# Optimization experiments

Measured on AMD Instinct MI355X. Metric: run time of the kernel, lower is better.

The kernel has to match this reference:

```python
import jax, jax.numpy as jnp
import numpy as np

N_NODES = 50000
N_EDGES = 640000
RAW = 128
HID = 256
COORD = 3


def setup_inputs() -> dict:
    key = jax.random.key(0)
    ks = jax.random.split(key, 20)

    def w(k, fan_in, fan_out):
        return (jax.random.normal(k, (fan_in, fan_out), jnp.float32)
                / np.float32(np.sqrt(fan_in)))

    return {
        "edge_index": jax.random.randint(ks[0], (2, N_EDGES), 0, N_NODES, jnp.int64)
        if jax.config.jax_enable_x64 else
        jax.random.randint(ks[0], (2, N_EDGES), 0, N_NODES, jnp.int32),
        "str_feature": jax.random.normal(ks[1], (N_NODES, RAW), jnp.float32),
        "coord_feature": jax.random.normal(ks[2], (N_NODES, COORD), jnp.float32),
        # msg_mlp: Linear(2*RAW+1 -> HID), SiLU, Linear(HID -> HID), SiLU
        "msg_w1": w(ks[3], 2 * RAW + 1, HID), "msg_b1": jnp.zeros((HID,), jnp.float32),
        "msg_w2": w(ks[4], HID, HID), "msg_b2": jnp.zeros((HID,), jnp.float32),
        # trans_mlp: Linear(HID->HID), SiLU, Linear(HID->HID), SiLU, Linear(HID->1, no bias, xavier gain=0.001)
        "tr_w1": w(ks[5], HID, HID), "tr_b1": jnp.zeros((HID,), jnp.float32),
        "tr_w2": w(ks[6], HID, HID), "tr_b2": jnp.zeros((HID,), jnp.float32),
        "tr_w3": w(ks[7], HID, 1) * np.float32(0.001),
        # posi_mlp: Linear(RAW+HID->HID), SiLU, Linear(HID->RAW)
        "posi_w1": w(ks[8], RAW + HID, HID), "posi_b1": jnp.zeros((HID,), jnp.float32),
        "posi_w2": w(ks[9], HID, RAW), "posi_b2": jnp.zeros((RAW,), jnp.float32),
    }


def reference(edge_index, str_feature, coord_feature,
              msg_w1, msg_b1, msg_w2, msg_b2,
              tr_w1, tr_b1, tr_w2, tr_b2, tr_w3,
              posi_w1, posi_b1, posi_w2, posi_b2):
    silu = jax.nn.silu
    row, col = edge_index[0], edge_index[1]
    n = str_feature.shape[0]

    # coord2dist
    coord_diff = coord_feature[row] - coord_feature[col]          # [E, 3]
    sqr_dist = jnp.sum(coord_diff * coord_diff, axis=1, keepdims=True)  # [E, 1]

    # msg_model
    edge_in = jnp.concatenate([str_feature[row], str_feature[col], sqr_dist], axis=1)
    msg = silu(silu(edge_in @ msg_w1 + msg_b1) @ msg_w2 + msg_b2)  # [E, HID]

    # coord_model: trans = coord_diff * trans_mlp(msg); x += segment_mean(trans, row)
    gate = silu(silu(msg @ tr_w1 + tr_b1) @ tr_w2 + tr_b2) @ tr_w3  # [E, 1]
    trans = coord_diff * gate                                       # [E, 3]
    trans_sum = jax.ops.segment_sum(trans, row, num_segments=n)     # [N, 3]
    cnt = jax.ops.segment_sum(jnp.ones((trans.shape[0],), trans.dtype), row,
                              num_segments=n)
    trans_mean = trans_sum / jnp.clip(cnt, 1.0)[:, None]
    coord_out = coord_feature + trans_mean

    # posi_model: p + posi_mlp([p, segment_sum(msg, row)])
    msg_sum = jax.ops.segment_sum(msg, row, num_segments=n)         # [N, HID]
    p_in = jnp.concatenate([str_feature, msg_sum], axis=1)
    str_out = str_feature + (silu(p_in @ posi_w1 + posi_b1) @ posi_w2 + posi_b2)

    return str_out, coord_out
```

## Files before the change

kernel.cpp:

```cpp
#include <hip/hip_runtime.h>

#define NN 50000
#define NE 640000

typedef __bf16 bf16x8 __attribute__((ext_vector_type(8)));
typedef short  short8 __attribute__((ext_vector_type(8)));
typedef float  f32x16 __attribute__((ext_vector_type(16)));
typedef float  f32x2  __attribute__((ext_vector_type(2)));
typedef float  f32x4  __attribute__((ext_vector_type(4)));

__device__ __forceinline__ short f2bf(float v) {
  unsigned u = __builtin_bit_cast(unsigned, v);
  u = (u + 0x7FFFu + ((u >> 16) & 1u)) >> 16;
  return (short)u;
}
__device__ __forceinline__ short f2bf_hw(float v) {
  return __builtin_bit_cast(short, (__bf16)v);
}
__device__ __forceinline__ float silu_f(float v) {
  float e = __builtin_amdgcn_exp2f(v * -1.44269504f);
  return v * __builtin_amdgcn_rcpf(1.0f + e);
}
__device__ __forceinline__ bf16x8 ld8(const short* p) {
  return *(const bf16x8*)(p);
}
__device__ __forceinline__ void atomic_add_f(float* p, float v) {
  __hip_atomic_fetch_add(p, v, __ATOMIC_RELAXED, __HIP_MEMORY_SCOPE_AGENT);
}

__global__ void egcl_prep(const float* __restrict__ mw1, const float* __restrict__ mb1,
                          const float* __restrict__ mw2, const float* __restrict__ mb2,
                          const float* __restrict__ tw1, const float* __restrict__ tb1,
                          const float* __restrict__ tw2, const float* __restrict__ tb2,
                          const float* __restrict__ pw1, const float* __restrict__ pw2,
                          const float* __restrict__ strf, const int* __restrict__ rowp,
                          short* __restrict__ w1t, short* __restrict__ w2t,
                          short* __restrict__ t1t, short* __restrict__ t2t,
                          short* __restrict__ p1t, short* __restrict__ p2t,
                          short* __restrict__ strb, int* __restrict__ deg)
{
  const int S0 = 71680, S2 = 98304, S3 = 32768, SS = NN * 128;
  const int total = 4 * S0 + S2 + S3 + SS + NE;
  int stride = gridDim.x * blockDim.x;
  for (int i = blockIdx.x * blockDim.x + threadIdx.x; i < total; i += stride) {
    int j = i;
    if (j < S0) { int n = j / 280, k = j - n * 280;
      float v = (k < 257) ? mw1[k * 256 + n] : ((k == 257) ? mb1[n] : 0.0f);
      w1t[j] = f2bf(v); continue; }
    j -= S0;
    if (j < S0) { int n = j / 280, k = j - n * 280;
      float v = (k < 256) ? mw2[k * 256 + n] : ((k == 257) ? mb2[n] : 0.0f);
      w2t[j] = f2bf(v); continue; }
    j -= S0;
    if (j < S0) { int n = j / 280, k = j - n * 280;
      float v = (k < 256) ? tw1[k * 256 + n] : ((k == 257) ? tb1[n] : 0.0f);
      t1t[j] = f2bf(v); continue; }
    j -= S0;
    if (j < S0) { int n = j / 280, k = j - n * 280;
      float v = (k < 256) ? tw2[k * 256 + n] : ((k == 257) ? tb2[n] : 0.0f);
      t2t[j] = f2bf(v); continue; }
    j -= S0;
    if (j < S2) { int n = j / 384, k = j - n * 384; p1t[j] = f2bf(pw1[k * 256 + n]); continue; }
    j -= S2;
    if (j < S3) { int n = j >> 8, k = j & 255; p2t[j] = f2bf(pw2[k * 128 + n]); continue; }
    j -= S3;
    if (j < SS) { strb[j] = f2bf(strf[j]); continue; }
    j -= SS;
    atomicAdd(deg + rowp[j], 1);
  }
}

__global__ __launch_bounds__(1024)
void egcl_scan(const int* __restrict__ deg, int* __restrict__ base)
{
  __shared__ int wsum[16], wincl[16];
  __shared__ int carry_s;
  const int tid = threadIdx.x, lane = tid & 63, w = tid >> 6;
  if (tid == 0) carry_s = 0;
  __syncthreads();
  for (int start = 0; start < NN; start += 1024) {
    const int i = start + tid;
    int v = (i < NN) ? deg[i] : 0;
    int s = v;
#pragma unroll
    for (int off = 1; off < 64; off <<= 1) {
      int t = __shfl_up(s, off);
      if (lane >= off) s += t;
    }
    if (lane == 63) wsum[w] = s;
    __syncthreads();
    if (w == 0) {
      int u = (lane < 16) ? wsum[lane] : 0;
#pragma unroll
      for (int off = 1; off < 16; off <<= 1) {
        int t = __shfl_up(u, off);
        if (lane >= off) u += t;
      }
      if (lane < 16) wincl[lane] = u;
    }
    __syncthreads();
    const int waveoff = wincl[w] - wsum[w];
    const int carry = carry_s;
    if (i < NN) base[i] = carry + waveoff + s - v;
    __syncthreads();
    if (tid == 0) carry_s = carry + wincl[15];
    __syncthreads();
  }
  if (tid == 0) base[NN] = NE;
}

__global__ void egcl_scatter(const int* __restrict__ rowp, const int* __restrict__ base,
                             int* __restrict__ cursor, int* __restrict__ eidg)
{
  int stride = gridDim.x * blockDim.x;
  for (int e = blockIdx.x * blockDim.x + threadIdx.x; e < NE; e += stride) {
    int r = rowp[e];
    int pos = base[r] + atomicAdd(cursor + r, 1);
    eidg[pos] = e;
  }
}


template<int NKS>
__device__ __forceinline__ void gemm64(const short* Ab, const short* __restrict__ WT,
                                       int wn, int lh, int l32, f32x16 acc[4])
{
  acc[0] = (f32x16)(0.0f); acc[1] = (f32x16)(0.0f);
  acc[2] = (f32x16)(0.0f); acc[3] = (f32x16)(0.0f);
  const short* arow = Ab + l32 * 280 + lh * 8;
  const short* brow = WT + (wn * 64 + l32) * 280 + lh * 8;
#pragma unroll
  for (int ks = 0; ks < NKS; ++ks) {
    const int kb = ks * 16;
    bf16x8 b0 = ld8(brow + kb);
    bf16x8 b1 = ld8(brow + 32 * 280 + kb);
    bf16x8 a0 = ld8(arow + kb);
    bf16x8 a1 = ld8(arow + 32 * 280 + kb);
    acc[0] = __builtin_amdgcn_mfma_f32_32x32x16_bf16(a0, b0, acc[0], 0, 0, 0);
    acc[1] = __builtin_amdgcn_mfma_f32_32x32x16_bf16(a1, b0, acc[1], 0, 0, 0);
    acc[2] = __builtin_amdgcn_mfma_f32_32x32x16_bf16(a0, b1, acc[2], 0, 0, 0);
    acc[3] = __builtin_amdgcn_mfma_f32_32x32x16_bf16(a1, b1, acc[3], 0, 0, 0);
  }
}

__device__ __forceinline__ void silu_acc(f32x16 acc[4], float b0, float b1)
{
#pragma unroll
  for (int i = 0; i < 4; ++i) {
    const float b = (i < 2) ? b0 : b1;
#pragma unroll
    for (int r = 0; r < 16; ++r) acc[i][r] = silu_f(acc[i][r] + b);
  }
}

__device__ __forceinline__ void write_acc(short* Ab, const f32x16 acc[4],
                                          int wn, int lh, int l32)
{
#pragma unroll
  for (int nh = 0; nh < 2; ++nh) {
    const int n = wn * 64 + nh * 32 + l32;
#pragma unroll
    for (int sm = 0; sm < 2; ++sm) {
      const f32x16& a = acc[nh * 2 + sm];
      short* dst = Ab + (sm * 32 + 4 * lh) * 280 + n;
#pragma unroll
      for (int j = 0; j < 8; ++j) {
        const int row = (j & 1) * 2 + 8 * (j >> 1);
        dst[row * 280]       = f2bf_hw(a[2 * j]);
        dst[(row + 1) * 280] = f2bf_hw(a[2 * j + 1]);
      }
    }
  }
}

__global__ __launch_bounds__(256, 4)
void egcl_edge(const int* __restrict__ eidx, const float* __restrict__ coord,
               const short* __restrict__ strb, const int* __restrict__ eidg,
               const int* __restrict__ base,
               const short* __restrict__ w1t, const short* __restrict__ w2t,
               const short* __restrict__ t1t, const short* __restrict__ t2t,
               const float* __restrict__ mb2v, const float* __restrict__ tb1v,
               const float* __restrict__ tb2v,
               const float* __restrict__ tr_w3,
               float* __restrict__ msg_sum, float* __restrict__ trans_sum)
{
  __shared__ short Ab[64 * 280];
  __shared__ int   rs_s[64], own_s[64];
  __shared__ float cdx_s[64], cdy_s[64], cdz_s[64], gate_s[64];

  const int tid  = threadIdx.x;
  const int lane = tid & 63, wave = tid >> 6;
  const int lh = lane >> 5, l32 = lane & 31;
  const int wn = wave;
  const int p0 = blockIdx.x * 64;
  const int* __restrict__ rowp = eidx;
  const int* __restrict__ colp = eidx + NE;

  const int nb = wn * 64 + l32;
  const float b2_0 = mb2v[nb], b2_1 = mb2v[nb + 32];
  const float b3_0 = tb1v[nb], b3_1 = tb1v[nb + 32];
  const float b4_0 = tb2v[nb], b4_1 = tb2v[nb + 32];

  if (tid < 64) {
    int e = eidg[p0 + tid];
    int r = rowp[e], c = colp[e];
    rs_s[tid] = r;
    const int wstart = p0 + (tid & ~31);
    own_s[tid] = (base[r] >= wstart) && (base[r + 1] <= wstart + 32) ? 1 : 0;
    float dx = coord[r * 3 + 0] - coord[c * 3 + 0];
    float dy = coord[r * 3 + 1] - coord[c * 3 + 1];
    float dz = coord[r * 3 + 2] - coord[c * 3 + 2];
    cdx_s[tid] = dx; cdy_s[tid] = dy; cdz_s[tid] = dz;
    short8 d8 = (short8)(short)0;
    d8[0] = f2bf(dx * dx + dy * dy + dz * dz);
    d8[1] = f2bf(1.0f);
    *(short8*)(Ab + tid * 280 + 256) = d8;
    *(short8*)(Ab + tid * 280 + 264) = (short8)(short)0;
    *(short8*)(Ab + tid * 280 + 272) = (short8)(short)0;
  }
#pragma unroll
  for (int it = 0; it < 8; ++it) {
    int i = tid + it * 256;
    int e = i >> 5, cc = i & 31;
    int eid = eidg[p0 + e];
    int node = (cc < 16) ? rowp[eid] : colp[eid];
    short8 v = *(const short8*)(strb + node * 128 + (cc & 15) * 8);
    *(short8*)(Ab + e * 280 + cc * 8) = v;
  }
  __syncthreads();

  f32x16 acc[4];

  gemm64<17>(Ab, w1t, wn, lh, l32, acc);
  silu_acc(acc, 0.0f, 0.0f);
  __syncthreads();
  write_acc(Ab, acc, wn, lh, l32);
  __syncthreads();

  gemm64<16>(Ab, w2t, wn, lh, l32, acc);
  silu_acc(acc, b2_0, b2_1);
  __syncthreads();
  write_acc(Ab, acc, wn, lh, l32);
  __syncthreads();

  gemm64<16>(Ab, t1t, wn, lh, l32, acc);
  silu_acc(acc, b3_0, b3_1);
  {
    const int cp  = tid & 127;
    const int e0w = (tid >> 7) * 32;
    float run0 = 0.0f, run1 = 0.0f;
    int prev = rs_s[e0w];
    int own  = own_s[e0w];
#pragma unroll 4
    for (int i = 0; i < 32; ++i) {
      const int idx = e0w + i;
      const int r = rs_s[idx];
      unsigned u = *(const unsigned*)(Ab + idx * 280 + cp * 2);
      float lo = __builtin_bit_cast(float, u << 16);
      float hi = __builtin_bit_cast(float, u & 0xFFFF0000u);
      if (r != prev) {
        if (own) {
          f32x2 v; v.x = run0; v.y = run1;
          *((f32x2*)msg_sum + prev * 128 + cp) = v;
        } else {
          atomic_add_f(msg_sum + prev * 256 + cp * 2 + 0, run0);
          atomic_add_f(msg_sum + prev * 256 + cp * 2 + 1, run1);
        }
        run0 = 0.0f; run1 = 0.0f; prev = r; own = own_s[idx];
      }
      run0 += lo; run1 += hi;
    }
    if (own) {
      f32x2 v; v.x = run0; v.y = run1;
      *((f32x2*)msg_sum + prev * 128 + cp) = v;
    } else {
      atomic_add_f(msg_sum + prev * 256 + cp * 2 + 0, run0);
      atomic_add_f(msg_sum + prev * 256 + cp * 2 + 1, run1);
    }
  }
  __syncthreads();
  write_acc(Ab, acc, wn, lh, l32);
  __syncthreads();

  gemm64<16>(Ab, t2t, wn, lh, l32, acc);
  silu_acc(acc, b4_0, b4_1);
  __syncthreads();
  write_acc(Ab, acc, wn, lh, l32);
  __syncthreads();

  {
    const int e = tid >> 2, p = tid & 3;
    const short* ap = Ab + e * 280 + p * 64;
    const float4* wp = (const float4*)(tr_w3 + p * 64);
    float s = 0.0f;
#pragma unroll
    for (int j = 0; j < 8; ++j) {
      bf16x8 av = ld8(ap + j * 8);
      float4 w0 = wp[2 * j], w1 = wp[2 * j + 1];
      s += (float)av[0] * w0.x + (float)av[1] * w0.y + (float)av[2] * w0.z + (float)av[3] * w0.w;
      s += (float)av[4] * w1.x + (float)av[5] * w1.y + (float)av[6] * w1.z + (float)av[7] * w1.w;
    }
    s += __shfl_xor(s, 1);
    s += __shfl_xor(s, 2);
    if (p == 0) gate_s[e] = s;
  }
  __syncthreads();
  if (tid < 64) {
    const int r = rs_s[tid];
    const float g = gate_s[tid];
    float vx = cdx_s[tid] * g, vy = cdy_s[tid] * g, vz = cdz_s[tid] * g;
#pragma unroll
    for (int off = 1; off < 64; off <<= 1) {
      int   rr = __shfl_up(r, off);
      float tx = __shfl_up(vx, off);
      float ty = __shfl_up(vy, off);
      float tz = __shfl_up(vz, off);
      if (tid >= off && rr == r) { vx += tx; vy += ty; vz += tz; }
    }
    int rn = __shfl_down(r, 1);
    if (tid == 63 || rn != r) {
      atomic_add_f(trans_sum + r * 3 + 0, vx);
      atomic_add_f(trans_sum + r * 3 + 1, vy);
      atomic_add_f(trans_sum + r * 3 + 2, vz);
    }
  }
}

__global__ __launch_bounds__(256, 3)
void egcl_node(const float* __restrict__ strf, const float* __restrict__ coord,
               const short* __restrict__ strb,
               const short* __restrict__ p1t, const short* __restrict__ p2t,
               const float* __restrict__ pb1, const float* __restrict__ pb2,
               const float* __restrict__ msg_sum, const float* __restrict__ trans_sum,
               const int* __restrict__ base, float* __restrict__ out)
{
  __shared__ short Ab[64 * 392];
  const int tid  = threadIdx.x;
  const int lane = tid & 63, wave = tid >> 6;
  const int quad = lane >> 4, l16 = lane & 15;
  const int n0 = blockIdx.x * 64;

#pragma unroll
  for (int it = 0; it < 4; ++it) {
    int i = tid + it * 256;
    int m = i >> 4, c = i & 15;
    int n = n0 + m;
    short8 v = (short8)(short)0;
    if (n < NN) v = *(const short8*)(strb + n * 128 + c * 8);
    *(short8*)(Ab + m * 392 + c * 8) = v;
  }
#pragma unroll
  for (int it = 0; it < 8; ++it) {
    int i = tid + it * 256;
    int m = i >> 5, c = i & 31;
    int n = n0 + m;
    short8 v = (short8)(short)0;
    if (n < NN) {
      const float* src = msg_sum + n * 256 + c * 8;
#pragma unroll
      for (int j = 0; j < 8; ++j) v[j] = f2bf_hw(src[j]);
    }
    *(short8*)(Ab + m * 392 + 128 + c * 8) = v;
  }
  __syncthreads();

  f32x4 acc[4][4];
#pragma unroll
  for (int nt = 0; nt < 4; ++nt)
#pragma unroll
    for (int mt = 0; mt < 4; ++mt) acc[nt][mt] = (f32x4)(0.0f);
#pragma unroll
  for (int ks = 0; ks < 12; ++ks) {
    const int kb = ks * 32 + quad * 8;
    bf16x8 b[4];
#pragma unroll
    for (int nt = 0; nt < 4; ++nt)
      b[nt] = ld8(p1t + (wave * 64 + nt * 16 + l16) * 384 + kb);
#pragma unroll
    for (int mt = 0; mt < 4; ++mt) {
      bf16x8 a = ld8(Ab + (mt * 16 + l16) * 392 + kb);
#pragma unroll
      for (int nt = 0; nt < 4; ++nt)
        acc[nt][mt] = __builtin_amdgcn_mfma_f32_16x16x32_bf16(a, b[nt], acc[nt][mt], 0, 0, 0);
    }
  }
  __syncthreads();
#pragma unroll
  for (int nt = 0; nt < 4; ++nt) {
    const int n = wave * 64 + nt * 16 + l16;
    const float bn = pb1[n];
#pragma unroll
    for (int mt = 0; mt < 4; ++mt)
#pragma unroll
      for (int r = 0; r < 4; ++r) {
        const int m = mt * 16 + quad * 4 + r;
        Ab[m * 392 + n] = f2bf_hw(silu_f(acc[nt][mt][r] + bn));
      }
  }
  __syncthreads();

  f32x4 a2[2][4];
#pragma unroll
  for (int nt = 0; nt < 2; ++nt)
#pragma unroll
    for (int mt = 0; mt < 4; ++mt) a2[nt][mt] = (f32x4)(0.0f);
#pragma unroll
  for (int ks = 0; ks < 8; ++ks) {
    const int kb = ks * 32 + quad * 8;
    bf16x8 b0 = ld8(p2t + (wave * 32 + l16) * 256 + kb);
    bf16x8 b1 = ld8(p2t + (wave * 32 + 16 + l16) * 256 + kb);
#pragma unroll
    for (int mt = 0; mt < 4; ++mt) {
      bf16x8 a = ld8(Ab + (mt * 16 + l16) * 392 + kb);
      a2[0][mt] = __builtin_amdgcn_mfma_f32_16x16x32_bf16(a, b0, a2[0][mt], 0, 0, 0);
      a2[1][mt] = __builtin_amdgcn_mfma_f32_16x16x32_bf16(a, b1, a2[1][mt], 0, 0, 0);
    }
  }
#pragma unroll
  for (int nt = 0; nt < 2; ++nt) {
    const int c = wave * 32 + nt * 16 + l16;
    const float bc = pb2[c];
#pragma unroll
    for (int mt = 0; mt < 4; ++mt)
#pragma unroll
      for (int r = 0; r < 4; ++r) {
        const int m = mt * 16 + quad * 4 + r;
        const int n = n0 + m;
        if (n < NN) out[n * 128 + c] = strf[n * 128 + c] + a2[nt][mt][r] + bc;
      }
  }
  if (tid < 64) {
    const int n = n0 + tid;
    if (n < NN) {
      float cv = (float)(base[n + 1] - base[n]); if (cv < 1.0f) cv = 1.0f;
      float inv = __builtin_amdgcn_rcpf(cv);
      out[NN * 128 + n * 3 + 0] = coord[n * 3 + 0] + trans_sum[n * 3 + 0] * inv;
      out[NN * 128 + n * 3 + 1] = coord[n * 3 + 1] + trans_sum[n * 3 + 1] * inv;
      out[NN * 128 + n * 3 + 2] = coord[n * 3 + 2] + trans_sum[n * 3 + 2] * inv;
    }
  }
}

extern "C" void kernel_launch(void* const* d_in, const int* in_sizes, int n_in,
                              void* d_out, int out_size, void* d_ws, size_t ws_size,
                              hipStream_t stream)
{
  const int*   eidx   = (const int*)d_in[0];
  const float* strf   = (const float*)d_in[1];
  const float* coord  = (const float*)d_in[2];
  const float* msg_w1 = (const float*)d_in[3];
  const float* msg_b1 = (const float*)d_in[4];
  const float* msg_w2 = (const float*)d_in[5];
  const float* msg_b2 = (const float*)d_in[6];
  const float* tr_w1  = (const float*)d_in[7];
  const float* tr_b1  = (const float*)d_in[8];
  const float* tr_w2  = (const float*)d_in[9];
  const float* tr_b2  = (const float*)d_in[10];
  const float* tr_w3  = (const float*)d_in[11];
  const float* posi_w1 = (const float*)d_in[12];
  const float* posi_b1 = (const float*)d_in[13];
  const float* posi_w2 = (const float*)d_in[14];
  const float* posi_b2 = (const float*)d_in[15];
  float* out = (float*)d_out;

  char* ws = (char*)d_ws;
  float* msg_sum   = (float*)ws;
  float* trans_sum = msg_sum + NN * 256;
  int*   deg       = (int*)(trans_sum + NN * 3);
  int*   cursor    = deg + NN;
  int*   base      = cursor + NN;
  int*   eidg      = base + NN + 8;
  short* strb = (short*)(eidg + NE);
  short* w1t  = strb + NN * 128;
  short* w2t  = w1t + 71680;
  short* t1t  = w2t + 71680;
  short* t2t  = t1t + 71680;
  short* p1t  = t2t + 71680;
  short* p2t  = p1t + 98304;

  const int* rowp = eidx;

  (void)hipMemsetAsync(ws, 0, (size_t)(NN * 256 + NN * 3 + NN + NN) * 4, stream);
  egcl_prep<<<2048, 256, 0, stream>>>(msg_w1, msg_b1, msg_w2, msg_b2,
                                      tr_w1, tr_b1, tr_w2, tr_b2,
                                      posi_w1, posi_w2,
                                      strf, rowp, w1t, w2t, t1t, t2t, p1t, p2t, strb, deg);
  egcl_scan<<<1, 1024, 0, stream>>>(deg, base);
  egcl_scatter<<<2560, 256, 0, stream>>>(rowp, base, cursor, eidg);
  egcl_edge<<<NE / 64, 256, 0, stream>>>(eidx, coord, strb, eidg, base,
                                         w1t, w2t, t1t, t2t,
                                         msg_b2, tr_b1, tr_b2, tr_w3,
                                         msg_sum, trans_sum);
  egcl_node<<<(NN + 63) / 64, 256, 0, stream>>>(strf, coord, strb, p1t, p2t,
                                                posi_b1, posi_b2,
                                                msg_sum, trans_sum, base, out);
}
```

Measured before the change: 1.040 ms.

## Retile edge MLP GEMMs to 2x2 waves with register-held A fragments

```diff
diff --git a/kernel.cpp b/kernel.cpp
--- a/kernel.cpp
+++ b/kernel.cpp
@@ -49,15 +49,15 @@
       w1t[j] = f2bf(v); continue; }
     j -= S0;
     if (j < S0) { int n = j / 280, k = j - n * 280;
-      float v = (k < 256) ? mw2[k * 256 + n] : ((k == 257) ? mb2[n] : 0.0f);
+      float v = (k < 256) ? mw2[k * 256 + n] : 0.0f;
       w2t[j] = f2bf(v); continue; }
     j -= S0;
     if (j < S0) { int n = j / 280, k = j - n * 280;
-      float v = (k < 256) ? tw1[k * 256 + n] : ((k == 257) ? tb1[n] : 0.0f);
+      float v = (k < 256) ? tw1[k * 256 + n] : 0.0f;
       t1t[j] = f2bf(v); continue; }
     j -= S0;
     if (j < S0) { int n = j / 280, k = j - n * 280;
-      float v = (k < 256) ? tw2[k * 256 + n] : ((k == 257) ? tb2[n] : 0.0f);
+      float v = (k < 256) ? tw2[k * 256 + n] : 0.0f;
       t2t[j] = f2bf(v); continue; }
     j -= S0;
     if (j < S2) { int n = j / 384, k = j - n * 384; p1t[j] = f2bf(pw1[k * 256 + n]); continue; }
@@ -122,58 +122,59 @@
 
 
 template<int NKS>
-__device__ __forceinline__ void gemm64(const short* Ab, const short* __restrict__ WT,
-                                       int wn, int lh, int l32, f32x16 acc[4])
+__device__ __forceinline__ void loadA(const short* Ab, int wm, int lh, int l32,
+                                      bf16x8 af[NKS])
+{
+  const short* arow = Ab + (wm * 32 + l32) * 280 + lh * 8;
+#pragma unroll
+  for (int ks = 0; ks < NKS; ++ks) af[ks] = ld8(arow + ks * 16);
+}
+
+template<int NKS>
+__device__ __forceinline__ void gemmA(const bf16x8 af[NKS], const short* __restrict__ WT,
+                                      int wn2, int lh, int l32, f32x16 acc[4])
 {
   acc[0] = (f32x16)(0.0f); acc[1] = (f32x16)(0.0f);
   acc[2] = (f32x16)(0.0f); acc[3] = (f32x16)(0.0f);
-  const short* arow = Ab + l32 * 280 + lh * 8;
-  const short* brow = WT + (wn * 64 + l32) * 280 + lh * 8;
+  const short* brow = WT + (wn2 * 128 + l32) * 280 + lh * 8;
 #pragma unroll
   for (int ks = 0; ks < NKS; ++ks) {
     const int kb = ks * 16;
     bf16x8 b0 = ld8(brow + kb);
     bf16x8 b1 = ld8(brow + 32 * 280 + kb);
-    bf16x8 a0 = ld8(arow + kb);
-    bf16x8 a1 = ld8(arow + 32 * 280 + kb);
-    acc[0] = __builtin_amdgcn_mfma_f32_32x32x16_bf16(a0, b0, acc[0], 0, 0, 0);
-    acc[1] = __builtin_amdgcn_mfma_f32_32x32x16_bf16(a1, b0, acc[1], 0, 0, 0);
-    acc[2] = __builtin_amdgcn_mfma_f32_32x32x16_bf16(a0, b1, acc[2], 0, 0, 0);
-    acc[3] = __builtin_amdgcn_mfma_f32_32x32x16_bf16(a1, b1, acc[3], 0, 0, 0);
-  }
-}
-
-__device__ __forceinline__ void silu_acc(f32x16 acc[4], float b0, float b1)
-{
-#pragma unroll
-  for (int i = 0; i < 4; ++i) {
-    const float b = (i < 2) ? b0 : b1;
-#pragma unroll
-    for (int r = 0; r < 16; ++r) acc[i][r] = silu_f(acc[i][r] + b);
-  }
-}
-
-__device__ __forceinline__ void write_acc(short* Ab, const f32x16 acc[4],
-                                          int wn, int lh, int l32)
-{
-#pragma unroll
-  for (int nh = 0; nh < 2; ++nh) {
-    const int n = wn * 64 + nh * 32 + l32;
-#pragma unroll
-    for (int sm = 0; sm < 2; ++sm) {
-      const f32x16& a = acc[nh * 2 + sm];
-      short* dst = Ab + (sm * 32 + 4 * lh) * 280 + n;
-#pragma unroll
-      for (int j = 0; j < 8; ++j) {
-        const int row = (j & 1) * 2 + 8 * (j >> 1);
-        dst[row * 280]       = f2bf_hw(a[2 * j]);
-        dst[(row + 1) * 280] = f2bf_hw(a[2 * j + 1]);
-      }
-    }
-  }
-}
-
-__global__ __launch_bounds__(256, 4)
+    bf16x8 b2 = ld8(brow + 64 * 280 + kb);
+    bf16x8 b3 = ld8(brow + 96 * 280 + kb);
+    acc[0] = __builtin_amdgcn_mfma_f32_32x32x16_bf16(af[ks], b0, acc[0], 0, 0, 0);
+    acc[1] = __builtin_amdgcn_mfma_f32_32x32x16_bf16(af[ks], b1, acc[1], 0, 0, 0);
+    acc[2] = __builtin_amdgcn_mfma_f32_32x32x16_bf16(af[ks], b2, acc[2], 0, 0, 0);
+    acc[3] = __builtin_amdgcn_mfma_f32_32x32x16_bf16(af[ks], b3, acc[3], 0, 0, 0);
+  }
+}
+
+__device__ __forceinline__ void siluD(f32x16 acc[4], const float bv[4])
+{
+#pragma unroll
+  for (int nc = 0; nc < 4; ++nc)
+#pragma unroll
+    for (int r = 0; r < 16; ++r) acc[nc][r] = silu_f(acc[nc][r] + bv[nc]);
+}
+
+__device__ __forceinline__ void writeD(short* Ab, const f32x16 acc[4],
+                                       int wm, int wn2, int lh, int l32)
+{
+#pragma unroll
+  for (int nc = 0; nc < 4; ++nc) {
+    short* dst = Ab + (wm * 32 + 4 * lh) * 280 + wn2 * 128 + nc * 32 + l32;
+#pragma unroll
+    for (int j = 0; j < 8; ++j) {
+      const int row = (j & 1) * 2 + 8 * (j >> 1);
+      dst[row * 280]       = f2bf_hw(acc[nc][2 * j]);
+      dst[(row + 1) * 280] = f2bf_hw(acc[nc][2 * j + 1]);
+    }
+  }
+}
+
+__global__ __launch_bounds__(256, 2)
 void egcl_edge(const int* __restrict__ eidx, const float* __restrict__ coord,
                const short* __restrict__ strb, const int* __restrict__ eidg,
                const int* __restrict__ base,
@@ -185,26 +186,31 @@
                float* __restrict__ msg_sum, float* __restrict__ trans_sum)
 {
   __shared__ short Ab[64 * 280];
-  __shared__ int   rs_s[64], own_s[64];
+  __shared__ int   rs_s[64], cs_s[64], own_s[64];
   __shared__ float cdx_s[64], cdy_s[64], cdz_s[64], gate_s[64];
 
   const int tid  = threadIdx.x;
   const int lane = tid & 63, wave = tid >> 6;
   const int lh = lane >> 5, l32 = lane & 31;
-  const int wn = wave;
+  const int wm = wave & 1, wn2 = wave >> 1;
   const int p0 = blockIdx.x * 64;
   const int* __restrict__ rowp = eidx;
   const int* __restrict__ colp = eidx + NE;
 
-  const int nb = wn * 64 + l32;
-  const float b2_0 = mb2v[nb], b2_1 = mb2v[nb + 32];
-  const float b3_0 = tb1v[nb], b3_1 = tb1v[nb + 32];
-  const float b4_0 = tb2v[nb], b4_1 = tb2v[nb + 32];
+  const int nb0 = wn2 * 128 + l32;
+  float b2v[4], b3v[4], b4v[4], zb[4];
+#pragma unroll
+  for (int nc = 0; nc < 4; ++nc) {
+    b2v[nc] = mb2v[nb0 + nc * 32];
+    b3v[nc] = tb1v[nb0 + nc * 32];
+    b4v[nc] = tb2v[nb0 + nc * 32];
+    zb[nc] = 0.0f;
+  }
 
   if (tid < 64) {
     int e = eidg[p0 + tid];
     int r = rowp[e], c = colp[e];
-    rs_s[tid] = r;
+    rs_s[tid] = r; cs_s[tid] = c;
     const int wstart = p0 + (tid & ~31);
     own_s[tid] = (base[r] >= wstart) && (base[r + 1] <= wstart + 32) ? 1 : 0;
     float dx = coord[r * 3 + 0] - coord[c * 3 + 0];
@@ -218,36 +224,41 @@
     *(short8*)(Ab + tid * 280 + 264) = (short8)(short)0;
     *(short8*)(Ab + tid * 280 + 272) = (short8)(short)0;
   }
+  __syncthreads();
 #pragma unroll
   for (int it = 0; it < 8; ++it) {
     int i = tid + it * 256;
     int e = i >> 5, cc = i & 31;
-    int eid = eidg[p0 + e];
-    int node = (cc < 16) ? rowp[eid] : colp[eid];
+    int node = (cc < 16) ? rs_s[e] : cs_s[e];
     short8 v = *(const short8*)(strb + node * 128 + (cc & 15) * 8);
     *(short8*)(Ab + e * 280 + cc * 8) = v;
   }
   __syncthreads();
 
+  bf16x8 af[17];
   f32x16 acc[4];
 
-  gemm64<17>(Ab, w1t, wn, lh, l32, acc);
-  silu_acc(acc, 0.0f, 0.0f);
-  __syncthreads();
-  write_acc(Ab, acc, wn, lh, l32);
-  __syncthreads();
-
-  gemm64<16>(Ab, w2t, wn, lh, l32, acc);
-  silu_acc(acc, b2_0, b2_1);
-  __syncthreads();
-  write_acc(Ab, acc, wn, lh, l32);
-  __syncthreads();
-
-  gemm64<16>(Ab, t1t, wn, lh, l32, acc);
-  silu_acc(acc, b3_0, b3_1);
+  loadA<17>(Ab, wm, lh, l32, af);
+  __syncthreads();
+  gemmA<17>(af, w1t, wn2, lh, l32, acc);
+  siluD(acc, zb);
+  writeD(Ab, acc, wm, wn2, lh, l32);
+  __syncthreads();
+
+  loadA<16>(Ab, wm, lh, l32, af);
+  __syncthreads();
+  gemmA<16>(af, w2t, wn2, lh, l32, acc);
+  siluD(acc, b2v);
+  writeD(Ab, acc, wm, wn2, lh, l32);
+  __syncthreads();
+
+  loadA<16>(Ab, wm, lh, l32, af);
+  __syncthreads();
+  gemmA<16>(af, t1t, wn2, lh, l32, acc);
+  siluD(acc, b3v);
   {
-    const int cp  = tid & 127;
-    const int e0w = (tid >> 7) * 32;
+    const int cp  = wn2 * 64 + lane;
+    const int e0w = wm * 32;
     float run0 = 0.0f, run1 = 0.0f;
     int prev = rs_s[e0w];
     int own  = own_s[e0w];
@@ -278,14 +289,14 @@
       atomic_add_f(msg_sum + prev * 256 + cp * 2 + 1, run1);
     }
   }
-  __syncthreads();
-  write_acc(Ab, acc, wn, lh, l32);
-  __syncthreads();
-
-  gemm64<16>(Ab, t2t, wn, lh, l32, acc);
-  silu_acc(acc, b4_0, b4_1);
-  __syncthreads();
-  write_acc(Ab, acc, wn, lh, l32);
+  writeD(Ab, acc, wm, wn2, lh, l32);
+  __syncthreads();
+
+  loadA<16>(Ab, wm, lh, l32, af);
+  __syncthreads();
+  gemmA<16>(af, t2t, wn2, lh, l32, acc);
+  siluD(acc, b4v);
+  writeD(Ab, acc, wm, wn2, lh, l32);
   __syncthreads();
 
   {
```

After: 1.348 ms. 29.7% more time.

## Shrink edge tile to 32 edges, pack bf16 outputs, fuse gate projection into epilogue

Applied to the files above, without the earlier changes.

```diff
diff --git a/kernel.cpp b/kernel.cpp
--- a/kernel.cpp
+++ b/kernel.cpp
@@ -17,6 +17,9 @@
 __device__ __forceinline__ short f2bf_hw(float v) {
   return __builtin_bit_cast(short, (__bf16)v);
 }
+__device__ __forceinline__ unsigned pack2(float a, float b) {
+  return (unsigned)(unsigned short)f2bf_hw(a) | ((unsigned)(unsigned short)f2bf_hw(b) << 16);
+}
 __device__ __forceinline__ float silu_f(float v) {
   float e = __builtin_amdgcn_exp2f(v * -1.44269504f);
   return v * __builtin_amdgcn_rcpf(1.0f + e);
@@ -29,9 +32,8 @@
 }
 
 __global__ void egcl_prep(const float* __restrict__ mw1, const float* __restrict__ mb1,
-                          const float* __restrict__ mw2, const float* __restrict__ mb2,
-                          const float* __restrict__ tw1, const float* __restrict__ tb1,
-                          const float* __restrict__ tw2, const float* __restrict__ tb2,
+                          const float* __restrict__ mw2,
+                          const float* __restrict__ tw1, const float* __restrict__ tw2,
                           const float* __restrict__ pw1, const float* __restrict__ pw2,
                           const float* __restrict__ strf, const int* __restrict__ rowp,
                           short* __restrict__ w1t, short* __restrict__ w2t,
@@ -49,15 +51,15 @@
       w1t[j] = f2bf(v); continue; }
     j -= S0;
     if (j < S0) { int n = j / 280, k = j - n * 280;
-      float v = (k < 256) ? mw2[k * 256 + n] : ((k == 257) ? mb2[n] : 0.0f);
+      float v = (k < 256) ? mw2[k * 256 + n] : 0.0f;
       w2t[j] = f2bf(v); continue; }
     j -= S0;
     if (j < S0) { int n = j / 280, k = j - n * 280;
-      float v = (k < 256) ? tw1[k * 256 + n] : ((k == 257) ? tb1[n] : 0.0f);
+      float v = (k < 256) ? tw1[k * 256 + n] : 0.0f;
       t1t[j] = f2bf(v); continue; }
     j -= S0;
     if (j < S0) { int n = j / 280, k = j - n * 280;
-      float v = (k < 256) ? tw2[k * 256 + n] : ((k == 257) ? tb2[n] : 0.0f);
+      float v = (k < 256) ? tw2[k * 256 + n] : 0.0f;
       t2t[j] = f2bf(v); continue; }
     j -= S0;
     if (j < S2) { int n = j / 384, k = j - n * 384; p1t[j] = f2bf(pw1[k * 256 + n]); continue; }
@@ -122,58 +124,50 @@
 
 
 template<int NKS>
-__device__ __forceinline__ void gemm64(const short* Ab, const short* __restrict__ WT,
-                                       int wn, int lh, int l32, f32x16 acc[4])
-{
-  acc[0] = (f32x16)(0.0f); acc[1] = (f32x16)(0.0f);
-  acc[2] = (f32x16)(0.0f); acc[3] = (f32x16)(0.0f);
+__device__ __forceinline__ void gemm32(const short* Ab, const short* __restrict__ WT,
+                                       int wn, int nh, int lh, int l32, f32x16& acc)
+{
+  acc = (f32x16)(0.0f);
   const short* arow = Ab + l32 * 280 + lh * 8;
-  const short* brow = WT + (wn * 64 + l32) * 280 + lh * 8;
+  const short* brow = WT + (wn * 64 + nh * 32 + l32) * 280 + lh * 8;
 #pragma unroll
   for (int ks = 0; ks < NKS; ++ks) {
     const int kb = ks * 16;
-    bf16x8 b0 = ld8(brow + kb);
-    bf16x8 b1 = ld8(brow + 32 * 280 + kb);
+    bf16x8 b  = ld8(brow + kb);
     bf16x8 a0 = ld8(arow + kb);
-    bf16x8 a1 = ld8(arow + 32 * 280 + kb);
-    acc[0] = __builtin_amdgcn_mfma_f32_32x32x16_bf16(a0, b0, acc[0], 0, 0, 0);
-    acc[1] = __builtin_amdgcn_mfma_f32_32x32x16_bf16(a1, b0, acc[1], 0, 0, 0);
-    acc[2] = __builtin_amdgcn_mfma_f32_32x32x16_bf16(a0, b1, acc[2], 0, 0, 0);
-    acc[3] = __builtin_amdgcn_mfma_f32_32x32x16_bf16(a1, b1, acc[3], 0, 0, 0);
-  }
-}
-
-__device__ __forceinline__ void silu_acc(f32x16 acc[4], float b0, float b1)
-{
-#pragma unroll
-  for (int i = 0; i < 4; ++i) {
-    const float b = (i < 2) ? b0 : b1;
-#pragma unroll
-    for (int r = 0; r < 16; ++r) acc[i][r] = silu_f(acc[i][r] + b);
-  }
-}
-
-__device__ __forceinline__ void write_acc(short* Ab, const f32x16 acc[4],
-                                          int wn, int lh, int l32)
+    acc = __builtin_amdgcn_mfma_f32_32x32x16_bf16(a0, b, acc, 0, 0, 0);
+  }
+}
+
+__device__ __forceinline__ void comp_pack(const f32x16& acc, unsigned pk[8], float b)
+{
+#pragma unroll
+  for (int j = 0; j < 8; ++j) {
+    float v0 = silu_f(acc[2 * j] + b);
+    float v1 = silu_f(acc[2 * j + 1] + b);
+    pk[j] = pack2(v0, v1);
+  }
+}
+
+__device__ __forceinline__ void write_pk(short* Ab, const unsigned pk0[8],
+                                         const unsigned pk1[8],
+                                         int wn, int lh, int l32)
 {
 #pragma unroll
   for (int nh = 0; nh < 2; ++nh) {
-    const int n = wn * 64 + nh * 32 + l32;
-#pragma unroll
-    for (int sm = 0; sm < 2; ++sm) {
-      const f32x16& a = acc[nh * 2 + sm];
-      short* dst = Ab + (sm * 32 + 4 * lh) * 280 + n;
-#pragma unroll
-      for (int j = 0; j < 8; ++j) {
-        const int row = (j & 1) * 2 + 8 * (j >> 1);
-        dst[row * 280]       = f2bf_hw(a[2 * j]);
-        dst[(row + 1) * 280] = f2bf_hw(a[2 * j + 1]);
-      }
-    }
-  }
-}
-
-__global__ __launch_bounds__(256, 4)
+    const unsigned* pk = nh ? pk1 : pk0;
+    short* dst = Ab + (4 * lh) * 280 + wn * 64 + nh * 32 + l32;
+#pragma unroll
+    for (int j = 0; j < 8; ++j) {
+      const int row = (j & 1) * 2 + 8 * (j >> 1);
+      const unsigned u = pk[j];
+      dst[row * 280]       = (short)(u & 0xFFFFu);
+      dst[(row + 1) * 280] = (short)(u >> 16);
+    }
+  }
+}
+
+__global__ __launch_bounds__(256, 6)
 void egcl_edge(const int* __restrict__ eidx, const float* __restrict__ coord,
                const short* __restrict__ strb, const int* __restrict__ eidg,
                const int* __restrict__ base,
@@ -184,29 +178,29 @@
                const float* __restrict__ tr_w3,
                float* __restrict__ msg_sum, float* __restrict__ trans_sum)
 {
-  __shared__ short Ab[64 * 280];
-  __shared__ int   rs_s[64], own_s[64];
-  __shared__ float cdx_s[64], cdy_s[64], cdz_s[64], gate_s[64];
+  __shared__ short Ab[32 * 280];
+  __shared__ int   rs_s[32], cs_s[32], own_s[32];
+  __shared__ float cdx_s[32], cdy_s[32], cdz_s[32], gate_s[32];
 
   const int tid  = threadIdx.x;
   const int lane = tid & 63, wave = tid >> 6;
   const int lh = lane >> 5, l32 = lane & 31;
-  const int wn = wave;
-  const int p0 = blockIdx.x * 64;
+  const int p0 = blockIdx.x * 32;
   const int* __restrict__ rowp = eidx;
   const int* __restrict__ colp = eidx + NE;
 
-  const int nb = wn * 64 + l32;
-  const float b2_0 = mb2v[nb], b2_1 = mb2v[nb + 32];
-  const float b3_0 = tb1v[nb], b3_1 = tb1v[nb + 32];
-  const float b4_0 = tb2v[nb], b4_1 = tb2v[nb + 32];
-
-  if (tid < 64) {
+  const int nb0 = wave * 64 + l32;
+  const float b2_0 = mb2v[nb0], b2_1 = mb2v[nb0 + 32];
+  const float b3_0 = tb1v[nb0], b3_1 = tb1v[nb0 + 32];
+  const float b4_0 = tb2v[nb0], b4_1 = tb2v[nb0 + 32];
+  const float w3_0 = tr_w3[nb0], w3_1 = tr_w3[nb0 + 32];
+
+  if (tid < 32) {
     int e = eidg[p0 + tid];
     int r = rowp[e], c = colp[e];
-    rs_s[tid] = r;
-    const int wstart = p0 + (tid & ~31);
-    own_s[tid] = (base[r] >= wstart) && (base[r + 1] <= wstart + 32) ? 1 : 0;
+    rs_s[tid] = r; cs_s[tid] = c;
+    const int wstart = p0 + (tid & ~15);
+    own_s[tid] = (base[r] >= wstart) && (base[r + 1] <= wstart + 16) ? 1 : 0;
     float dx = coord[r * 3 + 0] - coord[c * 3 + 0];
     float dy = coord[r * 3 + 1] - coord[c * 3 + 1];
     float dz = coord[r * 3 + 2] - coord[c * 3 + 2];
@@ -218,41 +212,48 @@
     *(short8*)(Ab + tid * 280 + 264) = (short8)(short)0;
     *(short8*)(Ab + tid * 280 + 272) = (short8)(short)0;
   }
-#pragma unroll
-  for (int it = 0; it < 8; ++it) {
+  __syncthreads();
+#pragma unroll
+  for (int it = 0; it < 4; ++it) {
     int i = tid + it * 256;
     int e = i >> 5, cc = i & 31;
-    int eid = eidg[p0 + e];
-    int node = (cc < 16) ? rowp[eid] : colp[eid];
+    int node = (cc < 16) ? rs_s[e] : cs_s[e];
     short8 v = *(const short8*)(strb + node * 128 + (cc & 15) * 8);
     *(short8*)(Ab + e * 280 + cc * 8) = v;
   }
   __syncthreads();
 
-  f32x16 acc[4];
-
-  gemm64<17>(Ab, w1t, wn, lh, l32, acc);
-  silu_acc(acc, 0.0f, 0.0f);
-  __syncthreads();
-  write_acc(Ab, acc, wn, lh, l32);
-  __syncthreads();
-
-  gemm64<16>(Ab, w2t, wn, lh, l32, acc);
-  silu_acc(acc, b2_0, b2_1);
-  __syncthreads();
-  write_acc(Ab, acc, wn, lh, l32);
-  __syncthreads();
-
-  gemm64<16>(Ab, t1t, wn, lh, l32, acc);
-  silu_acc(acc, b3_0, b3_1);
+  f32x16 acc;
+  unsigned pk0[8], pk1[8];
+
+  gemm32<17>(Ab, w1t, wave, 0, lh, l32, acc);
+  comp_pack(acc, pk0, 0.0f);
+  gemm32<17>(Ab, w1t, wave, 1, lh, l32, acc);
+  comp_pack(acc, pk1, 0.0f);
+  __syncthreads();
+  write_pk(Ab, pk0, pk1, wave, lh, l32);
+  __syncthreads();
+
+  gemm32<16>(Ab, w2t, wave, 0, lh, l32, acc);
+  comp_pack(acc, pk0, b2_0);
+  gemm32<16>(Ab, w2t, wave, 1, lh, l32, acc);
+  comp_pack(acc, pk1, b2_1);
+  __syncthreads();
+  write_pk(Ab, pk0, pk1, wave, lh, l32);
+  __syncthreads();
+
+  gemm32<16>(Ab, t1t, wave, 0, lh, l32, acc);
+  comp_pack(acc, pk0, b3_0);
+  gemm32<16>(Ab, t1t, wave, 1, lh, l32, acc);
+  comp_pack(acc, pk1, b3_1);
   {
     const int cp  = tid & 127;
-    const int e0w = (tid >> 7) * 32;
+    const int e0w = (tid >> 7) * 16;
     float run0 = 0.0f, run1 = 0.0f;
     int prev = rs_s[e0w];
     int own  = own_s[e0w];
 #pragma unroll 4
-    for (int i = 0; i < 32; ++i) {
+    for (int i = 0; i < 16; ++i) {
       const int idx = e0w + i;
       const int r = rs_s[idx];
       unsigned u = *(const unsigned*)(Ab + idx * 280 + cp * 2);
@@ -279,38 +280,49 @@
     }
   }
   __syncthreads();
-  write_acc(Ab, acc, wn, lh, l32);
-  __syncthreads();
-
-  gemm64<16>(Ab, t2t, wn, lh, l32, acc);
-  silu_acc(acc, b4_0, b4_1);
-  __syncthreads();
-  write_acc(Ab, acc, wn, lh, l32);
-  __syncthreads();
-
+  write_pk(Ab, pk0, pk1, wave, lh, l32);
+  __syncthreads();
+
+  float pd[16];
+  gemm32<16>(Ab, t2t, wave, 0, lh, l32, acc);
+#pragma unroll
+  for (int r = 0; r < 16; ++r) pd[r] = silu_f(acc[r] + b4_0) * w3_0;
+  gemm32<16>(Ab, t2t, wave, 1, lh, l32, acc);
+#pragma unroll
+  for (int r = 0; r < 16; ++r) pd[r] += silu_f(acc[r] + b4_1) * w3_1;
+  __syncthreads();
   {
-    const int e = tid >> 2, p = tid & 3;
-    const short* ap = Ab + e * 280 + p * 64;
-    const float4* wp = (const float4*)(tr_w3 + p * 64);
+    float* AbF = (float*)Ab;
+    const int pcol = wave * 32 + l32;
+#pragma unroll
+    for (int r = 0; r < 16; ++r) {
+      const int m = (r & 3) + 8 * (r >> 2) + 4 * lh;
+      AbF[m * 140 + pcol] = pd[r];
+    }
+  }
+  __syncthreads();
+  {
+    const float* AbF = (const float*)Ab;
+    const int e = tid >> 3, p = tid & 7;
+    const float* ap = AbF + e * 140 + p * 16;
     float s = 0.0f;
 #pragma unroll
-    for (int j = 0; j < 8; ++j) {
-      bf16x8 av = ld8(ap + j * 8);
-      float4 w0 = wp[2 * j], w1 = wp[2 * j + 1];
-      s += (float)av[0] * w0.x + (float)av[1] * w0.y + (float)av[2] * w0.z + (float)av[3] * w0.w;
-      s += (float)av[4] * w1.x + (float)av[5] * w1.y + (float)av[6] * w1.z + (float)av[7] * w1.w;
+    for (int j = 0; j < 4; ++j) {
+      f32x4 v = *(const f32x4*)(ap + j * 4);
+      s += v.x + v.y + v.z + v.w;
     }
     s += __shfl_xor(s, 1);
     s += __shfl_xor(s, 2);
+    s += __shfl_xor(s, 4);
     if (p == 0) gate_s[e] = s;
   }
   __syncthreads();
-  if (tid < 64) {
+  if (tid < 32) {
     const int r = rs_s[tid];
     const float g = gate_s[tid];
     float vx = cdx_s[tid] * g, vy = cdy_s[tid] * g, vz = cdz_s[tid] * g;
 #pragma unroll
-    for (int off = 1; off < 64; off <<= 1) {
+    for (int off = 1; off < 32; off <<= 1) {
       int   rr = __shfl_up(r, off);
       float tx = __shfl_up(vx, off);
       float ty = __shfl_up(vy, off);
@@ -318,7 +330,7 @@
       if (tid >= off && rr == r) { vx += tx; vy += ty; vz += tz; }
     }
     int rn = __shfl_down(r, 1);
-    if (tid == 63 || rn != r) {
+    if (tid == 31 || rn != r) {
       atomic_add_f(trans_sum + r * 3 + 0, vx);
       atomic_add_f(trans_sum + r * 3 + 1, vy);
       atomic_add_f(trans_sum + r * 3 + 2, vz);
@@ -481,13 +493,13 @@
   const int* rowp = eidx;
 
   (void)hipMemsetAsync(ws, 0, (size_t)(NN * 256 + NN * 3 + NN + NN) * 4, stream);
-  egcl_prep<<<2048, 256, 0, stream>>>(msg_w1, msg_b1, msg_w2, msg_b2,
-                                      tr_w1, tr_b1, tr_w2, tr_b2,
+  egcl_prep<<<2048, 256, 0, stream>>>(msg_w1, msg_b1, msg_w2,
+                                      tr_w1, tr_w2,
                                       posi_w1, posi_w2,
                                       strf, rowp, w1t, w2t, t1t, t2t, p1t, p2t, strb, deg);
   egcl_scan<<<1, 1024, 0, stream>>>(deg, base);
   egcl_scatter<<<2560, 256, 0, stream>>>(rowp, base, cursor, eidg);
-  egcl_edge<<<NE / 64, 256, 0, stream>>>(eidx, coord, strb, eidg, base,
+  egcl_edge<<<NE / 32, 256, 0, stream>>>(eidx, coord, strb, eidg, base,
                                          w1t, w2t, t1t, t2t,
                                          msg_b2, tr_b1, tr_b2, tr_w3,
                                          msg_sum, trans_sum);
```

Measured after the change: 1.318 ms. +26.8%, slower.
